# Kernel tuning notes

Measured on AMD Instinct MI355X. Metric: run time of the kernel, lower is better.

The kernel has to match this reference:

```python
import jax, jax.numpy as jnp
import numpy as np

N = 100000        # num nodes
E = 1600000       # num edges (avg degree 16)
IN_DIM = 256
OUT_DIM = 64
NEG_SLOPE = 0.2
EPS = 1e-9


def setup_inputs() -> dict:
    key = jax.random.key(0)
    k1, k2, k3, k4 = jax.random.split(key, 4)
    node_features = jax.random.normal(k1, (N, IN_DIM), dtype=jnp.float32)
    edge_index = jax.random.randint(k2, (2, E), 0, N, dtype=jnp.int32)
    # learned params (xavier-ish scale)
    W = jax.random.normal(k3, (OUT_DIM, IN_DIM), dtype=jnp.float32) * (1.0 / np.sqrt(IN_DIM))
    attn = jax.random.normal(k4, (2 * OUT_DIM,), dtype=jnp.float32) * (1.0 / np.sqrt(2 * OUT_DIM))
    bias = jnp.zeros((OUT_DIM,), dtype=jnp.float32)
    return {"node_features": node_features, "edge_index": edge_index,
            "W": W, "attn": attn, "bias": bias}


def reference(node_features, edge_index, W, attn, bias):
    # h = linear(node_features)  [N, D]
    h = node_features @ W.T
    src, dst = edge_index[0], edge_index[1]
    # (cat(h_src, h_dst) * attn).sum(-1) == h_src @ attn[:D] + h_dst @ attn[D:]
    a_src = h @ attn[:OUT_DIM]   # [N]
    a_dst = h @ attn[OUT_DIM:]   # [N]
    e = a_src[src] + a_dst[dst]  # [E]
    e = jnp.where(e >= 0, e, NEG_SLOPE * e)  # leaky_relu
    # segment softmax over dst
    max_per_dst = jax.ops.segment_max(e, dst, num_segments=N)       # [N]
    exp_scores = jnp.exp(e - max_per_dst[dst])                       # [E]
    sum_per_dst = jax.ops.segment_sum(exp_scores, dst, num_segments=N)
    attention = exp_scores / (sum_per_dst[dst] + EPS)                # [E]
    # dropout: p=0 / eval mode -> identity
    msg = attention[:, None] * h[src]                                 # [E, D]
    out = jax.ops.segment_sum(msg, dst, num_segments=N)              # [N, D]
    return out + bias
```

## Files before the change

### kernel.cpp

```cpp
#include <hip/hip_runtime.h>
#include <math.h>

#define IN_DIM 256
#define OUT_DIM 64
#define NEG_SLOPE 0.2f
#define EPS_GAT 1e-9f


__global__ __launch_bounds__(128) void gat_k1_linear(
    const float* __restrict__ X, const float* __restrict__ W,
    const float* __restrict__ attn, float* __restrict__ h,
    float* __restrict__ a_s, float* __restrict__ a_d, int N)
{
    __shared__ float sX[32 * 132];
    __shared__ float sW[32 * 68];

    const int tid = threadIdx.x;
    const int tx = tid & 7;
    const int ty = tid >> 3;
    const int n0 = blockIdx.x * 128;

    const float4* X4 = (const float4*)X;
    const float4* W4 = (const float4*)W;

    float acc[8][8];
    #pragma unroll
    for (int i = 0; i < 8; ++i)
        #pragma unroll
        for (int j = 0; j < 8; ++j) acc[i][j] = 0.f;

    float as_r[8], ad_r[8];
    #pragma unroll
    for (int j = 0; j < 8; ++j) {
        as_r[j] = attn[tx * 8 + j];
        ad_r[j] = attn[OUT_DIM + tx * 8 + j];
    }

    const int xc4 = tid & 7;
    const int xr0 = tid >> 3;

    for (int k0 = 0; k0 < IN_DIM; k0 += 32) {
        const int k0c4 = k0 >> 2;
        __syncthreads();
        #pragma unroll
        for (int p = 0; p < 8; ++p) {
            const int row = p * 16 + xr0;
            int n = n0 + row; if (n >= N) n = N - 1;
            float4 v = X4[(size_t)n * 64 + k0c4 + xc4];
            const int kb = xc4 * 4;
            sX[(kb + 0) * 132 + row] = v.x;
            sX[(kb + 1) * 132 + row] = v.y;
            sX[(kb + 2) * 132 + row] = v.z;
            sX[(kb + 3) * 132 + row] = v.w;
        }
        #pragma unroll
        for (int p = 0; p < 4; ++p) {
            const int idx = p * 128 + tid;
            const int o = idx >> 3, c4 = idx & 7;
            float4 v = W4[(size_t)o * 64 + k0c4 + c4];
            const int kb = c4 * 4;
            sW[(kb + 0) * 68 + o] = v.x;
            sW[(kb + 1) * 68 + o] = v.y;
            sW[(kb + 2) * 68 + o] = v.z;
            sW[(kb + 3) * 68 + o] = v.w;
        }
        __syncthreads();
        #pragma unroll 2
        for (int kk = 0; kk < 32; ++kk) {
            const float4* xp = (const float4*)&sX[kk * 132 + ty * 8];
            const float4* wp = (const float4*)&sW[kk * 68 + tx * 8];
            float4 xa = xp[0], xb = xp[1];
            float4 wa = wp[0], wb = wp[1];
            float xv[8] = {xa.x, xa.y, xa.z, xa.w, xb.x, xb.y, xb.z, xb.w};
            float wv[8] = {wa.x, wa.y, wa.z, wa.w, wb.x, wb.y, wb.z, wb.w};
            #pragma unroll
            for (int i = 0; i < 8; ++i)
                #pragma unroll
                for (int j = 0; j < 8; ++j) acc[i][j] += xv[i] * wv[j];
        }
    }

    float4* h4 = (float4*)h;
    #pragma unroll
    for (int m = 0; m < 8; ++m) {
        const int n = n0 + ty * 8 + m;
        float vs = 0.f, vd = 0.f;
        #pragma unroll
        for (int j = 0; j < 8; ++j) { vs += acc[m][j] * as_r[j]; vd += acc[m][j] * ad_r[j]; }
        vs += __shfl_xor(vs, 1); vs += __shfl_xor(vs, 2); vs += __shfl_xor(vs, 4);
        vd += __shfl_xor(vd, 1); vd += __shfl_xor(vd, 2); vd += __shfl_xor(vd, 4);
        if (n < N) {
            float4 lo = {acc[m][0], acc[m][1], acc[m][2], acc[m][3]};
            float4 hi = {acc[m][4], acc[m][5], acc[m][6], acc[m][7]};
            h4[(size_t)n * 16 + tx * 2]     = lo;
            h4[(size_t)n * 16 + tx * 2 + 1] = hi;
            if (tx == 0) { a_s[n] = vs; a_d[n] = vd; }
        }
    }
}

__global__ __launch_bounds__(256) void gat_p1a_bhist(
    const int* __restrict__ dst, int* __restrict__ bucketCnt, int E, int NB)
{
    __shared__ int cnt[1024];
    const int tid = threadIdx.x;
    for (int i = tid; i < NB; i += 256) cnt[i] = 0;
    __syncthreads();
    const int gtid = blockIdx.x * 256 + tid;
    const int gsz  = gridDim.x * 256;
    const int E4 = E >> 2;
    const int4* d4 = (const int4*)dst;
    for (int i = gtid; i < E4; i += gsz) {
        int4 v = d4[i];
        atomicAdd(&cnt[v.x >> 8], 1);
        atomicAdd(&cnt[v.y >> 8], 1);
        atomicAdd(&cnt[v.z >> 8], 1);
        atomicAdd(&cnt[v.w >> 8], 1);
    }
    for (int i = (E4 << 2) + gtid; i < E; i += gsz)
        atomicAdd(&cnt[dst[i] >> 8], 1);
    __syncthreads();
    for (int i = tid; i < NB; i += 256)
        if (cnt[i]) atomicAdd(&bucketCnt[i], cnt[i]);
}

__global__ __launch_bounds__(1024) void gat_p1b_bscan(
    const int* __restrict__ bucketCnt, int* __restrict__ bucketBase,
    int* __restrict__ bucketCursor, int NB)
{
    __shared__ int wsum[16];
    const int t = threadIdx.x;
    const int lane = t & 63;
    const int wave = t >> 6;
    const int v = (t < NB) ? bucketCnt[t] : 0;
    int incl = v;
    #pragma unroll
    for (int off = 1; off < 64; off <<= 1) {
        int x = __shfl_up(incl, off);
        if (lane >= off) incl += x;
    }
    if (lane == 63) wsum[wave] = incl;
    __syncthreads();
    if (wave == 0) {
        int wv = (lane < 16) ? wsum[lane] : 0;
        int wincl = wv;
        #pragma unroll
        for (int off = 1; off < 16; off <<= 1) {
            int x = __shfl_up(wincl, off);
            if (lane >= off) wincl += x;
        }
        if (lane < 16) wsum[lane] = wincl - wv;
    }
    __syncthreads();
    if (t < NB) {
        const int excl = wsum[wave] + (incl - v);
        bucketBase[t] = excl;
        bucketCursor[t] = excl;
    }
}

__global__ __launch_bounds__(256) void gat_p1c_partition(
    const int* __restrict__ src, const int* __restrict__ dst,
    int* __restrict__ bucketCursor, unsigned* __restrict__ pairs, int E)
{
    __shared__ int cnt[1024];
    __shared__ int run[1024];
    const int tid = threadIdx.x;
    const int chunk = (E + gridDim.x - 1) / gridDim.x;
    const int beg = blockIdx.x * chunk;
    const int end = min(E, beg + chunk);

    for (int i = tid; i < 1024; i += 256) cnt[i] = 0;
    __syncthreads();
    for (int i = beg + tid; i < end; i += 256)
        atomicAdd(&cnt[dst[i] >> 8], 1);
    __syncthreads();
    for (int i = tid; i < 1024; i += 256) {
        const int c = cnt[i];
        run[i] = c ? atomicAdd(&bucketCursor[i], c) : 0;
    }
    __syncthreads();
    for (int i = beg + tid; i < end; i += 256) {
        const int d = dst[i];
        const int pos = atomicAdd(&run[d >> 8], 1);
        pairs[pos] = ((unsigned)(d & 255) << 24) | (unsigned)src[i];
    }
}

__global__ __launch_bounds__(256) void gat_p2_csr(
    const unsigned* __restrict__ pairs, const int* __restrict__ bucketBase,
    const int* __restrict__ bucketCnt, int* __restrict__ offsets,
    int* __restrict__ counts, int* __restrict__ sorted_src, int N)
{
    __shared__ int cnt[256];
    __shared__ int offAbs[256];
    __shared__ int wsum[4];
    const int b = blockIdx.x;
    const int t = threadIdx.x;
    const int base = bucketBase[b];
    const int ecnt = bucketCnt[b];

    cnt[t] = 0;
    __syncthreads();
    for (int i = base + t; i < base + ecnt; i += 256)
        atomicAdd(&cnt[pairs[i] >> 24], 1);
    __syncthreads();

    const int lane = t & 63;
    const int wave = t >> 6;
    const int v = cnt[t];
    int incl = v;
    #pragma unroll
    for (int off = 1; off < 64; off <<= 1) {
        int x = __shfl_up(incl, off);
        if (lane >= off) incl += x;
    }
    if (lane == 63) wsum[wave] = incl;
    __syncthreads();
    int wpre = 0;
    for (int w = 0; w < wave; ++w) wpre += wsum[w];
    const int abs0 = base + wpre + (incl - v);
    offAbs[t] = abs0;
    const int d = b * 256 + t;
    if (d < N) { offsets[d] = abs0; counts[d] = v; }
    __syncthreads();

    for (int i = base + t; i < base + ecnt; i += 256) {
        const unsigned pv = pairs[i];
        const int pos = atomicAdd(&offAbs[pv >> 24], 1);
        sorted_src[pos] = (int)(pv & 0xFFFFFFu);
    }
}

__global__ __launch_bounds__(256) void gat_k5_aggregate(
    const float* __restrict__ h, const int* __restrict__ sorted_src,
    const int* __restrict__ offsets, const int* __restrict__ counts,
    const float* __restrict__ a_s, const float* __restrict__ a_d,
    const float* __restrict__ bias, float* __restrict__ out, int N)
{
    const int wave = threadIdx.x >> 6, lane = threadIdx.x & 63;
    const int d = blockIdx.x * 4 + wave;
    if (d >= N) return;
    const int deg  = counts[d];
    const int base = offsets[d];
    const float ad = a_d[d];
    const int slot = lane >> 4, q = lane & 15;
    const float4* h4 = (const float4*)h;

    float4 acc = {0.f, 0.f, 0.f, 0.f};

    if (deg <= 64) {
        int s = 0; float e = -INFINITY;
        if (lane < deg) {
            s = sorted_src[base + lane];
            e = a_s[s] + ad;
            e = (e >= 0.f) ? e : NEG_SLOPE * e;
        }
        float m = e;
        #pragma unroll
        for (int off = 32; off; off >>= 1) m = fmaxf(m, __shfl_xor(m, off));
        float p = (lane < deg) ? __expf(e - m) : 0.f;
        float sum = p;
        #pragma unroll
        for (int off = 32; off; off >>= 1) sum += __shfl_xor(sum, off);
        const float w = p / (sum + EPS_GAT);
        for (int t0 = 0; t0 < deg; t0 += 4) {
            const float wg = __shfl(w, t0 + slot);
            const int  sid = __shfl(s, t0 + slot);
            float4 hv = h4[(size_t)sid * 16 + q];
            acc.x += wg * hv.x; acc.y += wg * hv.y;
            acc.z += wg * hv.z; acc.w += wg * hv.w;
        }
    } else {
        float m = -INFINITY;
        for (int j = lane; j < deg; j += 64) {
            float e = a_s[sorted_src[base + j]] + ad;
            e = (e >= 0.f) ? e : NEG_SLOPE * e;
            m = fmaxf(m, e);
        }
        #pragma unroll
        for (int off = 32; off; off >>= 1) m = fmaxf(m, __shfl_xor(m, off));
        float sum = 0.f;
        for (int j = lane; j < deg; j += 64) {
            float e = a_s[sorted_src[base + j]] + ad;
            e = (e >= 0.f) ? e : NEG_SLOPE * e;
            sum += __expf(e - m);
        }
        #pragma unroll
        for (int off = 32; off; off >>= 1) sum += __shfl_xor(sum, off);
        const float inv = 1.f / (sum + EPS_GAT);
        for (int j0 = 0; j0 < deg; j0 += 64) {
            int s = 0; float w = 0.f;
            if (j0 + lane < deg) {
                s = sorted_src[base + j0 + lane];
                float e = a_s[s] + ad;
                e = (e >= 0.f) ? e : NEG_SLOPE * e;
                w = __expf(e - m) * inv;
            }
            const int cnt = min(64, deg - j0);
            for (int t0 = 0; t0 < cnt; t0 += 4) {
                const float wg = __shfl(w, t0 + slot);
                const int  sid = __shfl(s, t0 + slot);
                float4 hv = h4[(size_t)sid * 16 + q];
                acc.x += wg * hv.x; acc.y += wg * hv.y;
                acc.z += wg * hv.z; acc.w += wg * hv.w;
            }
        }
    }

    acc.x += __shfl_xor(acc.x, 16); acc.x += __shfl_xor(acc.x, 32);
    acc.y += __shfl_xor(acc.y, 16); acc.y += __shfl_xor(acc.y, 32);
    acc.z += __shfl_xor(acc.z, 16); acc.z += __shfl_xor(acc.z, 32);
    acc.w += __shfl_xor(acc.w, 16); acc.w += __shfl_xor(acc.w, 32);

    if (slot == 0) {
        const float4* b4 = (const float4*)bias;
        float4 bv = b4[q];
        float4 o;
        o.x = acc.x + bv.x; o.y = acc.y + bv.y;
        o.z = acc.z + bv.z; o.w = acc.w + bv.w;
        ((float4*)out)[(size_t)d * 16 + q] = o;
    }
}

extern "C" void kernel_launch(void* const* d_in, const int* in_sizes, int n_in,
                              void* d_out, int out_size, void* d_ws, size_t ws_size,
                              hipStream_t stream)
{
    const float* X    = (const float*)d_in[0];
    const int*   EI   = (const int*)d_in[1];
    const float* W    = (const float*)d_in[2];
    const float* attn = (const float*)d_in[3];
    const float* bias = (const float*)d_in[4];
    float* out = (float*)d_out;

    const int N = in_sizes[0] / IN_DIM;
    const int E = in_sizes[1] / 2;
    const int* src = EI;
    const int* dst = EI + E;
    const int NB = (N + 255) >> 8;

    char* ws = (char*)d_ws;
    float* h      = (float*)ws; ws += (size_t)N * OUT_DIM * sizeof(float);
    float* a_s    = (float*)ws; ws += (size_t)N * sizeof(float);
    float* a_d    = (float*)ws; ws += (size_t)N * sizeof(float);
    int*   counts = (int*)ws;   ws += (size_t)N * sizeof(int);
    int*   offsets= (int*)ws;   ws += (size_t)N * sizeof(int);
    int*   bucketCnt    = (int*)ws; ws += 1024 * sizeof(int);
    int*   bucketBase   = (int*)ws; ws += 1024 * sizeof(int);
    int*   bucketCursor = (int*)ws; ws += 1024 * sizeof(int);
    unsigned* pairs     = (unsigned*)ws; ws += (size_t)E * sizeof(unsigned);
    int*   sorted_src   = (int*)ws;      ws += (size_t)E * sizeof(int);

    hipMemsetAsync(bucketCnt, 0, 1024 * sizeof(int), stream);

    gat_k1_linear<<<(N + 127) / 128, 128, 0, stream>>>(X, W, attn, h, a_s, a_d, N);
    gat_p1a_bhist<<<256, 256, 0, stream>>>(dst, bucketCnt, E, NB);
    gat_p1b_bscan<<<1, 1024, 0, stream>>>(bucketCnt, bucketBase, bucketCursor, NB);
    gat_p1c_partition<<<128, 256, 0, stream>>>(src, dst, bucketCursor, pairs, E);
    gat_p2_csr<<<NB, 256, 0, stream>>>(pairs, bucketBase, bucketCnt, offsets,
                                       counts, sorted_src, N);
    gat_k5_aggregate<<<(N + 3) / 4, 256, 0, stream>>>(h, sorted_src, offsets, counts,
                                                      a_s, a_d, bias, out, N);
}
```

Before: 350.7 us.

## Compute node linear projection with bf16x3 split MFMA instead of FP32 FMA

Replaces the shared-memory tiled FP32 GEMM for h = X·Wᵀ with a per-wave MFMA kernel. Each FP32 input is split into bf16 hi and lo parts, and three 16x16x32 bf16 MFMAs per fragment keep accuracy close to FP32. Operands are loaded straight from global memory without LDS staging, and the attention dot products are reduced with cross-lane shuffles. The trade-offs are extra split arithmetic, W being re-read by every wave, and uncoalesced scalar stores of h.

```diff
diff --git a/kernel.cpp b/kernel.cpp
--- a/kernel.cpp
+++ b/kernel.cpp
@@ -6,96 +6,87 @@
 #define NEG_SLOPE 0.2f
 #define EPS_GAT 1e-9f
 
-
-__global__ __launch_bounds__(128) void gat_k1_linear(
+typedef __attribute__((ext_vector_type(8))) short short8v;
+typedef __attribute__((ext_vector_type(4))) float float4v;
+
+
+struct bfrag { short8v hi, lo; };
+
+__device__ __forceinline__ bfrag split8(float4 a, float4 b) {
+    float f[8] = {a.x, a.y, a.z, a.w, b.x, b.y, b.z, b.w};
+    bfrag r;
+    #pragma unroll
+    for (int j = 0; j < 8; ++j) {
+        unsigned u = __float_as_uint(f[j]);
+        unsigned t = (u + 0x7FFFu + ((u >> 16) & 1u)) >> 16;
+        r.hi[j] = (short)t;
+        float rem = f[j] - __uint_as_float(t << 16);
+        r.lo[j] = (short)(__float_as_uint(rem) >> 16);
+    }
+    return r;
+}
+
+__global__ __launch_bounds__(256) void gat_k1_mfma(
     const float* __restrict__ X, const float* __restrict__ W,
     const float* __restrict__ attn, float* __restrict__ h,
     float* __restrict__ a_s, float* __restrict__ a_d, int N)
 {
-    __shared__ float sX[32 * 132];
-    __shared__ float sW[32 * 68];
-
-    const int tid = threadIdx.x;
-    const int tx = tid & 7;
-    const int ty = tid >> 3;
-    const int n0 = blockIdx.x * 128;
+    const int lane = threadIdx.x & 63;
+    const int gw = blockIdx.x * 4 + (threadIdx.x >> 6);
+    const int m0 = gw * 16;
+    if (m0 >= N) return;
+
+    const int row = lane & 15;
+    const int q   = lane >> 4;
+    const int kb  = q * 2;
 
     const float4* X4 = (const float4*)X;
     const float4* W4 = (const float4*)W;
 
-    float acc[8][8];
-    #pragma unroll
-    for (int i = 0; i < 8; ++i)
-        #pragma unroll
-        for (int j = 0; j < 8; ++j) acc[i][j] = 0.f;
-
-    float as_r[8], ad_r[8];
-    #pragma unroll
-    for (int j = 0; j < 8; ++j) {
-        as_r[j] = attn[tx * 8 + j];
-        ad_r[j] = attn[OUT_DIM + tx * 8 + j];
-    }
-
-    const int xc4 = tid & 7;
-    const int xr0 = tid >> 3;
-
+    const int rx = min(m0 + row, N - 1);
+
+    float at_s[4], at_d[4];
+    #pragma unroll
+    for (int nf = 0; nf < 4; ++nf) {
+        at_s[nf] = attn[nf * 16 + row];
+        at_d[nf] = attn[OUT_DIM + nf * 16 + row];
+    }
+
+    float4v acc[4];
+    #pragma unroll
+    for (int nf = 0; nf < 4; ++nf) acc[nf] = (float4v){0.f, 0.f, 0.f, 0.f};
+
+    #pragma unroll
     for (int k0 = 0; k0 < IN_DIM; k0 += 32) {
-        const int k0c4 = k0 >> 2;
-        __syncthreads();
-        #pragma unroll
-        for (int p = 0; p < 8; ++p) {
-            const int row = p * 16 + xr0;
-            int n = n0 + row; if (n >= N) n = N - 1;
-            float4 v = X4[(size_t)n * 64 + k0c4 + xc4];
-            const int kb = xc4 * 4;
-            sX[(kb + 0) * 132 + row] = v.x;
-            sX[(kb + 1) * 132 + row] = v.y;
-            sX[(kb + 2) * 132 + row] = v.z;
-            sX[(kb + 3) * 132 + row] = v.w;
-        }
-        #pragma unroll
-        for (int p = 0; p < 4; ++p) {
-            const int idx = p * 128 + tid;
-            const int o = idx >> 3, c4 = idx & 7;
-            float4 v = W4[(size_t)o * 64 + k0c4 + c4];
-            const int kb = c4 * 4;
-            sW[(kb + 0) * 68 + o] = v.x;
-            sW[(kb + 1) * 68 + o] = v.y;
-            sW[(kb + 2) * 68 + o] = v.z;
-            sW[(kb + 3) * 68 + o] = v.w;
-        }
-        __syncthreads();
-        #pragma unroll 2
-        for (int kk = 0; kk < 32; ++kk) {
-            const float4* xp = (const float4*)&sX[kk * 132 + ty * 8];
-            const float4* wp = (const float4*)&sW[kk * 68 + tx * 8];
-            float4 xa = xp[0], xb = xp[1];
-            float4 wa = wp[0], wb = wp[1];
-            float xv[8] = {xa.x, xa.y, xa.z, xa.w, xb.x, xb.y, xb.z, xb.w};
-            float wv[8] = {wa.x, wa.y, wa.z, wa.w, wb.x, wb.y, wb.z, wb.w};
-            #pragma unroll
-            for (int i = 0; i < 8; ++i)
-                #pragma unroll
-                for (int j = 0; j < 8; ++j) acc[i][j] += xv[i] * wv[j];
-        }
-    }
-
-    float4* h4 = (float4*)h;
-    #pragma unroll
-    for (int m = 0; m < 8; ++m) {
-        const int n = n0 + ty * 8 + m;
+        const int c4 = (k0 >> 2) + kb;
+        const float4* xp = X4 + (size_t)rx * 64 + c4;
+        bfrag af = split8(xp[0], xp[1]);
+        #pragma unroll
+        for (int nf = 0; nf < 4; ++nf) {
+            const float4* wp = W4 + (size_t)(nf * 16 + row) * 64 + c4;
+            bfrag bf = split8(wp[0], wp[1]);
+            acc[nf] = __builtin_amdgcn_mfma_f32_16x16x32_bf16(af.hi, bf.hi, acc[nf], 0, 0, 0);
+            acc[nf] = __builtin_amdgcn_mfma_f32_16x16x32_bf16(af.hi, bf.lo, acc[nf], 0, 0, 0);
+            acc[nf] = __builtin_amdgcn_mfma_f32_16x16x32_bf16(af.lo, bf.hi, acc[nf], 0, 0, 0);
+        }
+    }
+
+    #pragma unroll
+    for (int r = 0; r < 4; ++r) {
+        const int node = m0 + q * 4 + r;
         float vs = 0.f, vd = 0.f;
         #pragma unroll
-        for (int j = 0; j < 8; ++j) { vs += acc[m][j] * as_r[j]; vd += acc[m][j] * ad_r[j]; }
-        vs += __shfl_xor(vs, 1); vs += __shfl_xor(vs, 2); vs += __shfl_xor(vs, 4);
-        vd += __shfl_xor(vd, 1); vd += __shfl_xor(vd, 2); vd += __shfl_xor(vd, 4);
-        if (n < N) {
-            float4 lo = {acc[m][0], acc[m][1], acc[m][2], acc[m][3]};
-            float4 hi = {acc[m][4], acc[m][5], acc[m][6], acc[m][7]};
-            h4[(size_t)n * 16 + tx * 2]     = lo;
-            h4[(size_t)n * 16 + tx * 2 + 1] = hi;
-            if (tx == 0) { a_s[n] = vs; a_d[n] = vd; }
-        }
+        for (int nf = 0; nf < 4; ++nf) {
+            const float v = acc[nf][r];
+            if (node < N) h[(size_t)node * OUT_DIM + nf * 16 + row] = v;
+            vs += v * at_s[nf];
+            vd += v * at_d[nf];
+        }
+        vs += __shfl_xor(vs, 1); vs += __shfl_xor(vs, 2);
+        vs += __shfl_xor(vs, 4); vs += __shfl_xor(vs, 8);
+        vd += __shfl_xor(vd, 1); vd += __shfl_xor(vd, 2);
+        vd += __shfl_xor(vd, 4); vd += __shfl_xor(vd, 8);
+        if (row == 0 && node < N) { a_s[node] = vs; a_d[node] = vd; }
     }
 }
 
@@ -354,7 +345,8 @@
 
     hipMemsetAsync(bucketCnt, 0, 1024 * sizeof(int), stream);
 
-    gat_k1_linear<<<(N + 127) / 128, 128, 0, stream>>>(X, W, attn, h, a_s, a_d, N);
+    const int nwaves = (N + 15) / 16;
+    gat_k1_mfma<<<(nwaves + 3) / 4, 256, 0, stream>>>(X, W, attn, h, a_s, a_d, N);
     gat_p1a_bhist<<<256, 256, 0, stream>>>(dst, bucketCnt, E, NB);
     gat_p1b_bscan<<<1, 1024, 0, stream>>>(bucketCnt, bucketBase, bucketCursor, NB);
     gat_p1c_partition<<<128, 256, 0, stream>>>(src, dst, bucketCursor, pairs, E);
```

Result: no change. 354.4 us (+1.0%).
